# Kernel tuning notes

Measured on AMD Instinct MI355X. Metric: run time of the kernel, lower is better.

## Reference

```python
import jax, jax.numpy as jnp
import numpy as np

LORA_SCALE = 0.5
LAYER_IDX = 0
NUM_ADAPTERS = 8

def setup_inputs() -> dict:
    key = jax.random.key(0)
    ks = jax.random.split(key, 11)
    T, H, I, A, L, R = 2048, 4096, 11008, NUM_ADAPTERS, 1, 16
    s_base = 1.0 / np.sqrt(H)
    s_down = 1.0 / np.sqrt(I)
    return {
        "x": jax.random.normal(ks[0], (T, H), jnp.float32),
        "gate_w": jax.random.normal(ks[1], (I, H), jnp.float32) * s_base,
        "up_w": jax.random.normal(ks[2], (I, H), jnp.float32) * s_base,
        "down_w": jax.random.normal(ks[3], (H, I), jnp.float32) * s_down,
        "gate_wa": jax.random.normal(ks[4], (A, L, R, H), jnp.float32) * s_base,
        "gate_wb": jax.random.normal(ks[5], (A, L, I, R), jnp.float32) * 0.01,
        "up_wa": jax.random.normal(ks[6], (A, L, R, H), jnp.float32) * s_base,
        "up_wb": jax.random.normal(ks[7], (A, L, I, R), jnp.float32) * 0.01,
        "down_wa": jax.random.normal(ks[8], (A, L, R, I), jnp.float32) * s_down,
        "down_wb": jax.random.normal(ks[9], (A, L, H, R), jnp.float32) * 0.01,
        "indices": jax.random.randint(ks[10], (T,), 0, A, jnp.int64),
    }

def _add_lora(y, x_in, wa, wb, idx, scale):
    # wa: [A, L, r, in], wb: [A, L, out, r]; per-token adapter gather (BGMV)
    wa_t = wa[idx, LAYER_IDX]          # [T, r, in]
    wb_t = wb[idx, LAYER_IDX]          # [T, out, r]
    v = jnp.einsum('ti,tri->tr', x_in, wa_t)     # [T, r]
    return y + scale * jnp.einsum('tr,tor->to', v, wb_t)

def reference(x, gate_w, up_w, down_w, gate_wa, gate_wb, up_wa, up_wb, down_wa, down_wb, indices):
    gate = x @ gate_w.T                                   # [T, I]
    gate = _add_lora(gate, x, gate_wa, gate_wb, indices, LORA_SCALE)
    gate = jax.nn.silu(gate)
    up = x @ up_w.T                                       # [T, I]
    up = _add_lora(up, x, up_wa, up_wb, indices, LORA_SCALE)
    t = gate * up                                         # [T, I]
    down = t @ down_w.T                                   # [T, H]
    down = _add_lora(down, t, down_wa, down_wb, indices, LORA_SCALE)
    return down
```

## Files before the change

### kernel.cpp

```cpp
#include <hip/hip_runtime.h>
#include <hip/hip_bf16.h>
#include <cstdint>


#define T_TOK 2048
#define H_DIM 4096
#define I_DIM 11008
#define R_LORA 16
#define KA1 4352
#define KA2 11136
#define N_STK 22016

typedef __bf16 bf16x8 __attribute__((ext_vector_type(8)));
typedef float f32x4 __attribute__((ext_vector_type(4)));

__device__ __forceinline__ float bf2f(unsigned short u) {
    union { unsigned int i; float f; } v;
    v.i = ((unsigned int)u) << 16;
    return v.f;
}
__device__ __forceinline__ unsigned short f2bf(float f) {
    __bf16 b = (__bf16)f;
    unsigned short u;
    __builtin_memcpy(&u, &b, 2);
    return u;
}
__device__ __forceinline__ void cvt8(const float* s, unsigned short* d) {
    float4 a = reinterpret_cast<const float4*>(s)[0];
    float4 b = reinterpret_cast<const float4*>(s)[1];
    uint4 o;
    o.x = (unsigned)f2bf(a.x) | ((unsigned)f2bf(a.y) << 16);
    o.y = (unsigned)f2bf(a.z) | ((unsigned)f2bf(a.w) << 16);
    o.z = (unsigned)f2bf(b.x) | ((unsigned)f2bf(b.y) << 16);
    o.w = (unsigned)f2bf(b.z) | ((unsigned)f2bf(b.w) << 16);
    *reinterpret_cast<uint4*>(d) = o;
}
__device__ __forceinline__ void gload_lds16(const void* g, void* l) {
    __builtin_amdgcn_global_load_lds(
        (const __attribute__((address_space(1))) void*)g,
        (__attribute__((address_space(3))) void*)l,
        16, 0, 0);
}

__global__ __launch_bounds__(256) void cvt_rows(
    const float* __restrict__ src, unsigned short* __restrict__ dst, int K)
{
    const int row = blockIdx.x;
    const int tid = threadIdx.x;
    const float* s = src + (size_t)row * K;
    unsigned short* d = dst + (size_t)row * K;
    for (int k = tid * 8; k < K; k += 256 * 8) cvt8(s + k, d + k);
}

__global__ __launch_bounds__(256) void build_xa_x(
    const float* __restrict__ x, unsigned short* __restrict__ xa)
{
    const int t = blockIdx.x;
    const int tid = threadIdx.x;
    const float* s = x + (size_t)t * H_DIM;
    unsigned short* d = xa + (size_t)t * KA1;
    for (int k = tid * 8; k < H_DIM; k += 2048) cvt8(s + k, d + k);
}

__global__ __launch_bounds__(256) void fill_xa_aug(
    const float* __restrict__ P, const int* __restrict__ idx,
    unsigned short* __restrict__ xa)
{
    const int t = blockIdx.x;
    const int tid = threadIdx.x;
    const int a = (tid & 127) >> 4;
    float v = 0.f;
    if (a == idx[t]) {
        #pragma unroll
        for (int s = 0; s < 4; ++s)
            v += P[((size_t)s * T_TOK + t) * 256 + tid];
        v *= 0.5f;
    }
    xa[(size_t)t * KA1 + H_DIM + tid] = f2bf(v);
}

__global__ __launch_bounds__(128) void fill_ta(
    const float* __restrict__ P, const int* __restrict__ idx,
    unsigned short* __restrict__ t_aug)
{
    const int t = blockIdx.x;
    const int tid = threadIdx.x;
    const int a = tid >> 4;
    float v = 0.f;
    if (a == idx[t]) {
        #pragma unroll
        for (int s = 0; s < 4; ++s)
            v += P[((size_t)s * T_TOK + t) * 128 + tid];
        v *= 0.5f;
    }
    t_aug[(size_t)t * KA2 + I_DIM + tid] = f2bf(v);
}

__global__ __launch_bounds__(256) void build_w_aug(
    const float* __restrict__ w, const float* __restrict__ wb,
    unsigned short* __restrict__ dst,
    int Nrows, int Ksrc, int Kdst, int self_off, int zero_off)
{
    const int c = blockIdx.x;
    const int tid = threadIdx.x;
    const float* src = w + (size_t)c * Ksrc;
    unsigned short* d = dst + (size_t)c * Kdst;
    for (int k = tid * 8; k < Ksrc; k += 256 * 8) cvt8(src + k, d + k);
    if (tid < 128) {
        const int a = tid >> 4, r = tid & 15;
        const float v = wb[(((size_t)a * Nrows) + c) * R_LORA + r];
        d[self_off + tid] = f2bf(v);
        if (zero_off >= 0) d[zero_off + tid] = 0;
    }
}

__global__ __launch_bounds__(256) void silu_mul(
    const unsigned short* __restrict__ C, unsigned short* __restrict__ T)
{
    const long long nv = (long long)T_TOK * (I_DIM / 8);
    long long i = (long long)blockIdx.x * 256 + threadIdx.x;
    const long long stride = (long long)gridDim.x * 256;
    for (; i < nv; i += stride) {
        const int t = (int)(i / (I_DIM / 8));
        const int c8 = (int)(i % (I_DIM / 8)) * 8;
        const unsigned short* g = C + (size_t)t * N_STK + c8;
        uint4 gv = *reinterpret_cast<const uint4*>(g);
        uint4 uv = *reinterpret_cast<const uint4*>(g + I_DIM);
        const unsigned short* gp = reinterpret_cast<const unsigned short*>(&gv);
        const unsigned short* up = reinterpret_cast<const unsigned short*>(&uv);
        unsigned short og[8];
        #pragma unroll
        for (int e = 0; e < 8; ++e) {
            const float gf = bf2f(gp[e]);
            const float uf = bf2f(up[e]);
            og[e] = f2bf(uf * gf / (1.f + __expf(-gf)));
        }
        *reinterpret_cast<uint4*>(T + (size_t)t * KA2 + c8) =
            *reinterpret_cast<const uint4*>(og);
    }
}

__global__ __launch_bounds__(256) void add_inplace(
    float* __restrict__ out, const float* __restrict__ p)
{
    const long long n4 = (long long)T_TOK * H_DIM / 4;
    long long i = (long long)blockIdx.x * 256 + threadIdx.x;
    const long long stride = (long long)gridDim.x * 256;
    for (; i < n4; i += stride) {
        float4 a = reinterpret_cast<float4*>(out)[i];
        float4 b = reinterpret_cast<const float4*>(p)[i];
        a.x += b.x; a.y += b.y; a.z += b.z; a.w += b.w;
        reinterpret_cast<float4*>(out)[i] = a;
    }
}

__global__ __launch_bounds__(512) void gemm_thin_sk(
    const unsigned short* __restrict__ A, int lda,
    const unsigned short* __restrict__ B, int ldb,
    float* __restrict__ P, int N, int K)
{
    __shared__ __align__(16) unsigned short As[128][64];
    __shared__ __align__(16) unsigned short Bs[128][64];

    const int tid = threadIdx.x;
    const int lane = tid & 63;
    const int wid = tid >> 6;
    const int wr = wid >> 2;
    const int wc = wid & 3;
    const int fr = lane & 15;
    const int hi = lane >> 4;
    const int fsw = fr & 7;

    const int bm0 = blockIdx.y * 128;
    const int bn0 = blockIdx.x * 128;
    const int ks = K / 4;
    const int k0 = blockIdx.z * ks;
    float* out = P + (size_t)blockIdx.z * T_TOK * N;

    const int srow = tid >> 3;
    const int sslot = tid & 7;
    const int gcol = (sslot ^ (srow & 7)) * 8;
    const unsigned short* Ag = A + (size_t)(bm0 + srow) * lda + gcol;
    const unsigned short* Bg = B + (size_t)(bn0 + srow) * ldb + gcol;
    const size_t halfA = (size_t)64 * lda;
    const size_t halfB = (size_t)64 * ldb;

    f32x4 acc[4][2] = {};

    for (int kt = k0; kt < k0 + ks; kt += 64) {
        gload_lds16(Ag + kt,         &As[srow][sslot * 8]);
        gload_lds16(Ag + halfA + kt, &As[64 + srow][sslot * 8]);
        gload_lds16(Bg + kt,         &Bs[srow][sslot * 8]);
        gload_lds16(Bg + halfB + kt, &Bs[64 + srow][sslot * 8]);
        __syncthreads();
        #pragma unroll
        for (int kk = 0; kk < 2; ++kk) {
            bf16x8 a_[4], b_[2];
            #pragma unroll
            for (int m = 0; m < 4; ++m)
                a_[m] = *reinterpret_cast<const bf16x8*>(
                    &As[wr * 64 + m * 16 + fr][((kk * 4 + hi) ^ fsw) * 8]);
            #pragma unroll
            for (int n = 0; n < 2; ++n)
                b_[n] = *reinterpret_cast<const bf16x8*>(
                    &Bs[wc * 32 + n * 16 + fr][((kk * 4 + hi) ^ fsw) * 8]);
            #pragma unroll
            for (int m = 0; m < 4; ++m)
                #pragma unroll
                for (int n = 0; n < 2; ++n)
                    acc[m][n] = __builtin_amdgcn_mfma_f32_16x16x32_bf16(
                        a_[m], b_[n], acc[m][n], 0, 0, 0);
        }
        __syncthreads();
    }

    const int orow0 = bm0 + wr * 64 + hi * 4;
    const int ocol0 = bn0 + wc * 32 + fr;
    #pragma unroll
    for (int m = 0; m < 4; ++m)
        #pragma unroll
        for (int j = 0; j < 4; ++j) {
            const int row = orow0 + m * 16 + j;
            #pragma unroll
            for (int n = 0; n < 2; ++n)
                out[(size_t)row * N + ocol0 + n * 16] = acc[m][n][j];
        }
}

#define RD_A(BUF, MH)                                                         \
    do {                                                                      \
        _Pragma("unroll")                                                     \
        for (int mq = 0; mq < 4; ++mq) {                                      \
            _Pragma("unroll")                                                 \
            for (int k = 0; k < 2; ++k)                                       \
                a_[mq][k] = *reinterpret_cast<const bf16x8*>(                 \
                    &lds[BUF][wr * 128 + (MH) * 64 + mq * 16 + fr]            \
                        [((k * 4 + hi) ^ fsw) * 8]);                          \
        }                                                                     \
    } while (0)

#define RD_B(BUF, NH, DST)                                                    \
    do {                                                                      \
        _Pragma("unroll")                                                     \
        for (int nq = 0; nq < 2; ++nq) {                                      \
            _Pragma("unroll")                                                 \
            for (int k = 0; k < 2; ++k)                                       \
                DST[nq][k] = *reinterpret_cast<const bf16x8*>(                \
                    &lds[BUF][256 + wc * 64 + (NH) * 32 + nq * 16 + fr]       \
                        [((k * 4 + hi) ^ fsw) * 8]);                          \
        }                                                                     \
    } while (0)

#define MM(MH, NH, BSRC)                                                      \
    do {                                                                      \
        _Pragma("unroll")                                                     \
        for (int mq = 0; mq < 4; ++mq) {                                      \
            _Pragma("unroll")                                                 \
            for (int nq = 0; nq < 2; ++nq) {                                  \
                _Pragma("unroll")                                             \
                for (int k = 0; k < 2; ++k)                                   \
                    acc[(MH) * 4 + mq][(NH) * 2 + nq] =                       \
                        __builtin_amdgcn_mfma_f32_16x16x32_bf16(              \
                            a_[mq][k], BSRC[nq][k],                           \
                            acc[(MH) * 4 + mq][(NH) * 2 + nq], 0, 0, 0);      \
            }                                                                 \
        }                                                                     \
    } while (0)

template <int MODE>
__global__ __launch_bounds__(512, 2) void gemmk(
    const unsigned short* __restrict__ A, int lda,
    const unsigned short* __restrict__ B, int ldb,
    int nks_in,
    unsigned short* __restrict__ outb, int ldob,
    float* __restrict__ outf0, float* __restrict__ outf1)
{
    __shared__ __align__(16) unsigned short lds[2][512][64];

    const int tid = threadIdx.x;
    const int lane = tid & 63;
    const int wid = tid >> 6;
    const int wr = wid >> 2;
    const int wc = wid & 3;
    const int fr = lane & 15;
    const int hi = lane >> 4;
    const int fsw = fr & 7;

    int bm, bn, koff = 0, nks = nks_in;
    float* outf = outf0;
    if constexpr (MODE == 2) {
        bm = blockIdx.x & 7;
        bn = (blockIdx.x >> 3) & 15;
        nks = 87;
        if (blockIdx.x >> 7) { koff = 87 * 64; outf = outf1; }
    } else {
        bm = blockIdx.x & 7;
        bn = blockIdx.x >> 3;
    }
    const int bm0 = bm * 256;
    const int bn0 = bn * 256;

    const int srow = tid >> 3;
    const int sslot = tid & 7;
    const int gcol = (sslot ^ (srow & 7)) * 8;
    const unsigned short* Ap = A + (size_t)(bm0 + srow) * lda + gcol + koff;
    const unsigned short* Bp = B + (size_t)(bn0 + srow) * ldb + gcol + koff;

    f32x4 acc[8][4] = {};
    bf16x8 a_[4][2], b0_[2][2], b1_[2][2];

    auto stage = [&](int buf, int kt) {
        #pragma unroll
        for (int q = 0; q < 4; ++q)
            gload_lds16(Ap + (size_t)(q * 64) * lda + kt,
                        &lds[buf][q * 64 + srow][sslot * 8]);
        #pragma unroll
        for (int q = 0; q < 4; ++q)
            gload_lds16(Bp + (size_t)(q * 64) * ldb + kt,
                        &lds[buf][256 + q * 64 + srow][sslot * 8]);
    };

    stage(0, 0);
    __syncthreads();

    for (int t = 0; t < nks; ++t) {
        const int cur = t & 1;
        if (t + 1 < nks) stage(cur ^ 1, (t + 1) * 64);

        RD_A(cur, 0);
        RD_B(cur, 0, b0_);
        MM(0, 0, b0_);
        RD_B(cur, 1, b1_);
        MM(0, 1, b1_);
        RD_A(cur, 1);
        MM(1, 0, b0_);
        MM(1, 1, b1_);

        __syncthreads();
    }

    const int orow0 = bm0 + wr * 128 + hi * 4;
    const int ocol0 = bn0 + wc * 64 + fr;
    #pragma unroll
    for (int m = 0; m < 8; ++m) {
        #pragma unroll
        for (int jj = 0; jj < 4; ++jj) {
            const int row = orow0 + m * 16 + jj;
            #pragma unroll
            for (int n = 0; n < 4; ++n) {
                const int col = ocol0 + n * 16;
                if constexpr (MODE == 0) {
                    outb[(size_t)row * ldob + col] = f2bf(acc[m][n][jj]);
                } else if constexpr (MODE == 1) {
                    const float g = bf2f(outb[(size_t)row * ldob + col]);
                    const float u = acc[m][n][jj];
                    outb[(size_t)row * ldob + col] =
                        f2bf(u * g / (1.f + __expf(-g)));
                } else {
                    outf[(size_t)row * H_DIM + col] = acc[m][n][jj];
                }
            }
        }
    }
}

extern "C" void kernel_launch(void* const* d_in, const int* in_sizes, int n_in,
                              void* d_out, int out_size, void* d_ws, size_t ws_size,
                              hipStream_t stream)
{
    const float* x       = (const float*)d_in[0];
    const float* gate_w  = (const float*)d_in[1];
    const float* up_w    = (const float*)d_in[2];
    const float* down_w  = (const float*)d_in[3];
    const float* gate_wa = (const float*)d_in[4];
    const float* gate_wb = (const float*)d_in[5];
    const float* up_wa   = (const float*)d_in[6];
    const float* up_wb   = (const float*)d_in[7];
    const float* down_wa = (const float*)d_in[8];
    const float* down_wb = (const float*)d_in[9];
    const int*   indices = (const int*)d_in[10];
    float* out = (float*)d_out;

    char* ws = (char*)d_ws;
    size_t off = 0;
    auto alloc = [&](size_t bytes) {
        char* p = ws + off;
        off += (bytes + 255) & ~(size_t)255;
        return p;
    };
    unsigned short* xa     = (unsigned short*)alloc((size_t)T_TOK * KA1 * 2);
    unsigned short* wg_aug = (unsigned short*)alloc((size_t)I_DIM * KA1 * 2);
    unsigned short* wu_aug = (unsigned short*)alloc((size_t)I_DIM * KA1 * 2);
    unsigned short* t_aug  = (unsigned short*)alloc((size_t)T_TOK * KA2 * 2);
    unsigned short* wab_gu = (unsigned short*)alloc((size_t)256 * H_DIM * 2);
    const size_t base_need = off;
    const size_t c_need = ((size_t)T_TOK * N_STK * 2 + 255) & ~(size_t)255;
    const bool stacked = (ws_size >= base_need + c_need);
    unsigned short* Cbuf = stacked ? (unsigned short*)alloc(c_need) : nullptr;

    float* Pgu = (float*)(t_aug);
    float* Pd  = stacked ? (float*)Cbuf
                         : (float*)(t_aug + (size_t)T_TOK * KA2) - (size_t)T_TOK * 128 * 4;
    unsigned short* wd_aug = wu_aug;
    unsigned short* wab_d  = wu_aug + (size_t)H_DIM * KA2;
    float* partial1 = (float*)wg_aug;

    cvt_rows<<<128, 256, 0, stream>>>(gate_wa, wab_gu, H_DIM);
    cvt_rows<<<128, 256, 0, stream>>>(up_wa, wab_gu + (size_t)128 * H_DIM, H_DIM);
    build_xa_x<<<T_TOK, 256, 0, stream>>>(x, xa);
    gemm_thin_sk<<<dim3(2, 16, 4), 512, 0, stream>>>(xa, KA1, wab_gu, H_DIM, Pgu, 256, H_DIM);
    fill_xa_aug<<<T_TOK, 256, 0, stream>>>(Pgu, indices, xa);

    build_w_aug<<<I_DIM, 256, 0, stream>>>(gate_w, gate_wb, wg_aug,
                                           I_DIM, H_DIM, KA1, H_DIM, H_DIM + 128);
    build_w_aug<<<I_DIM, 256, 0, stream>>>(up_w, up_wb, wu_aug,
                                           I_DIM, H_DIM, KA1, H_DIM + 128, H_DIM);

    if (stacked) {
        gemmk<0><<<8 * (N_STK / 256), 512, 0, stream>>>(
            xa, KA1, wg_aug, KA1, KA1 / 64, Cbuf, N_STK, nullptr, nullptr);
        silu_mul<<<2048, 256, 0, stream>>>(Cbuf, t_aug);
    } else {
        gemmk<0><<<8 * (I_DIM / 256), 512, 0, stream>>>(
            xa, KA1, wg_aug, KA1, KA1 / 64, t_aug, KA2, nullptr, nullptr);
        gemmk<1><<<8 * (I_DIM / 256), 512, 0, stream>>>(
            xa, KA1, wu_aug, KA1, KA1 / 64, t_aug, KA2, nullptr, nullptr);
    }

    cvt_rows<<<128, 256, 0, stream>>>(down_wa, wab_d, I_DIM);
    gemm_thin_sk<<<dim3(1, 16, 4), 512, 0, stream>>>(t_aug, KA2, wab_d, I_DIM, Pd, 128, I_DIM);
    fill_ta<<<T_TOK, 128, 0, stream>>>(Pd, indices, t_aug);
    build_w_aug<<<H_DIM, 256, 0, stream>>>(down_w, down_wb, wd_aug,
                                           H_DIM, I_DIM, KA2, I_DIM, -1);

    gemmk<2><<<256, 512, 0, stream>>>(
        t_aug, KA2, wd_aug, KA2, 0, nullptr, 0, out, partial1);
    add_inplace<<<2048, 256, 0, stream>>>(out, partial1);

    (void)in_sizes; (void)n_in; (void)out_size; (void)ws_size;
}
```

Measured before the change: 837.4 us.

## Interleave gate/up weight rows and fuse SiLU-multiply into GEMM epilogue

Gate and up weight rows are interleaved into one stacked B matrix so each output column pair (gate, up) lands in adjacent lanes. The GEMM epilogue exchanges the pair with a lane shuffle and writes silu(gate)*up directly into t_aug. This removes the stacked bf16 intermediate buffer, the separate silu_mul pass and one of the two weight-build launches. The down-projection split-K block mapping is also remapped per XCD, and the workspace layout is reworked. Half the lanes sit idle during the epilogue store, and the stores are strided.

After: 816.2 us. -2.5%, faster.

```diff
diff --git a/kernel.cpp b/kernel.cpp
--- a/kernel.cpp
+++ b/kernel.cpp
@@ -96,10 +96,31 @@
     t_aug[(size_t)t * KA2 + I_DIM + tid] = f2bf(v);
 }
 
+__global__ __launch_bounds__(256) void build_w_int(
+    const float* __restrict__ gw, const float* __restrict__ uw,
+    const float* __restrict__ gwb, const float* __restrict__ uwb,
+    unsigned short* __restrict__ dst)
+{
+    const int c = blockIdx.x;
+    const int i = c >> 1;
+    const int par = c & 1;
+    const int tid = threadIdx.x;
+    const float* src = (par ? uw : gw) + (size_t)i * H_DIM;
+    const float* wb  = (par ? uwb : gwb);
+    unsigned short* d = dst + (size_t)c * KA1;
+    for (int k = tid * 8; k < H_DIM; k += 256 * 8) cvt8(src + k, d + k);
+    if (tid < 128) {
+        const int a = tid >> 4, r = tid & 15;
+        const float v = wb[(((size_t)a * I_DIM) + i) * R_LORA + r];
+        d[H_DIM + par * 128 + tid] = f2bf(v);
+        d[H_DIM + (1 - par) * 128 + tid] = 0;
+    }
+}
+
 __global__ __launch_bounds__(256) void build_w_aug(
     const float* __restrict__ w, const float* __restrict__ wb,
     unsigned short* __restrict__ dst,
-    int Nrows, int Ksrc, int Kdst, int self_off, int zero_off)
+    int Nrows, int Ksrc, int Kdst, int self_off)
 {
     const int c = blockIdx.x;
     const int tid = threadIdx.x;
@@ -110,33 +131,6 @@
         const int a = tid >> 4, r = tid & 15;
         const float v = wb[(((size_t)a * Nrows) + c) * R_LORA + r];
         d[self_off + tid] = f2bf(v);
-        if (zero_off >= 0) d[zero_off + tid] = 0;
-    }
-}
-
-__global__ __launch_bounds__(256) void silu_mul(
-    const unsigned short* __restrict__ C, unsigned short* __restrict__ T)
-{
-    const long long nv = (long long)T_TOK * (I_DIM / 8);
-    long long i = (long long)blockIdx.x * 256 + threadIdx.x;
-    const long long stride = (long long)gridDim.x * 256;
-    for (; i < nv; i += stride) {
-        const int t = (int)(i / (I_DIM / 8));
-        const int c8 = (int)(i % (I_DIM / 8)) * 8;
-        const unsigned short* g = C + (size_t)t * N_STK + c8;
-        uint4 gv = *reinterpret_cast<const uint4*>(g);
-        uint4 uv = *reinterpret_cast<const uint4*>(g + I_DIM);
-        const unsigned short* gp = reinterpret_cast<const unsigned short*>(&gv);
-        const unsigned short* up = reinterpret_cast<const unsigned short*>(&uv);
-        unsigned short og[8];
-        #pragma unroll
-        for (int e = 0; e < 8; ++e) {
-            const float gf = bf2f(gp[e]);
-            const float uf = bf2f(up[e]);
-            og[e] = f2bf(uf * gf / (1.f + __expf(-gf)));
-        }
-        *reinterpret_cast<uint4*>(T + (size_t)t * KA2 + c8) =
-            *reinterpret_cast<const uint4*>(og);
     }
 }
 
@@ -272,7 +266,7 @@
     const unsigned short* __restrict__ A, int lda,
     const unsigned short* __restrict__ B, int ldb,
     int nks_in,
-    unsigned short* __restrict__ outb, int ldob,
+    unsigned short* __restrict__ outb,
     float* __restrict__ outf0, float* __restrict__ outf1)
 {
     __shared__ __align__(16) unsigned short lds[2][512][64];
@@ -289,10 +283,12 @@
     int bm, bn, koff = 0, nks = nks_in;
     float* outf = outf0;
     if constexpr (MODE == 2) {
-        bm = blockIdx.x & 7;
-        bn = (blockIdx.x >> 3) & 15;
+        const int xcd = blockIdx.x & 7;
+        const int c = blockIdx.x >> 3;
+        bm = (xcd >> 1) * 2 + (c & 1);
+        bn = (xcd & 1) * 8 + ((c >> 1) & 7);
         nks = 87;
-        if (blockIdx.x >> 7) { koff = 87 * 64; outf = outf1; }
+        if (c >> 4) { koff = 87 * 64; outf = outf1; }
     } else {
         bm = blockIdx.x & 7;
         bn = blockIdx.x >> 3;
@@ -348,16 +344,16 @@
             const int row = orow0 + m * 16 + jj;
             #pragma unroll
             for (int n = 0; n < 4; ++n) {
-                const int col = ocol0 + n * 16;
-                if constexpr (MODE == 0) {
-                    outb[(size_t)row * ldob + col] = f2bf(acc[m][n][jj]);
-                } else if constexpr (MODE == 1) {
-                    const float g = bf2f(outb[(size_t)row * ldob + col]);
-                    const float u = acc[m][n][jj];
-                    outb[(size_t)row * ldob + col] =
-                        f2bf(u * g / (1.f + __expf(-g)));
+                if constexpr (MODE == 3) {
+                    const float v = acc[m][n][jj];
+                    const float w = __shfl_xor(v, 1);
+                    if ((fr & 1) == 0) {
+                        const float sg = v / (1.f + __expf(-v));
+                        const int s = ocol0 + n * 16;
+                        outb[(size_t)row * KA2 + (s >> 1)] = f2bf(sg * w);
+                    }
                 } else {
-                    outf[(size_t)row * H_DIM + col] = acc[m][n][jj];
+                    outf[(size_t)row * H_DIM + ocol0 + n * 16] = acc[m][n][jj];
                 }
             }
         }
@@ -388,22 +384,16 @@
         off += (bytes + 255) & ~(size_t)255;
         return p;
     };
-    unsigned short* xa     = (unsigned short*)alloc((size_t)T_TOK * KA1 * 2);
-    unsigned short* wg_aug = (unsigned short*)alloc((size_t)I_DIM * KA1 * 2);
-    unsigned short* wu_aug = (unsigned short*)alloc((size_t)I_DIM * KA1 * 2);
-    unsigned short* t_aug  = (unsigned short*)alloc((size_t)T_TOK * KA2 * 2);
+    unsigned short* xa    = (unsigned short*)alloc((size_t)T_TOK * KA1 * 2);
+    unsigned short* wB    = (unsigned short*)alloc((size_t)N_STK * KA1 * 2);
+    unsigned short* t_aug = (unsigned short*)alloc((size_t)T_TOK * KA2 * 2);
     unsigned short* wab_gu = (unsigned short*)alloc((size_t)256 * H_DIM * 2);
-    const size_t base_need = off;
-    const size_t c_need = ((size_t)T_TOK * N_STK * 2 + 255) & ~(size_t)255;
-    const bool stacked = (ws_size >= base_need + c_need);
-    unsigned short* Cbuf = stacked ? (unsigned short*)alloc(c_need) : nullptr;
-
-    float* Pgu = (float*)(t_aug);
-    float* Pd  = stacked ? (float*)Cbuf
-                         : (float*)(t_aug + (size_t)T_TOK * KA2) - (size_t)T_TOK * 128 * 4;
-    unsigned short* wd_aug = wu_aug;
-    unsigned short* wab_d  = wu_aug + (size_t)H_DIM * KA2;
-    float* partial1 = (float*)wg_aug;
+
+    float* Pgu = (float*)t_aug;
+    float* Pd  = (float*)xa;
+    unsigned short* wd_aug = wB;
+    unsigned short* wab_d  = wB + (size_t)H_DIM * KA2;
+    float* partial1 = (float*)(wab_d + (size_t)128 * I_DIM + 64);
 
     cvt_rows<<<128, 256, 0, stream>>>(gate_wa, wab_gu, H_DIM);
     cvt_rows<<<128, 256, 0, stream>>>(up_wa, wab_gu + (size_t)128 * H_DIM, H_DIM);
@@ -411,30 +401,19 @@
     gemm_thin_sk<<<dim3(2, 16, 4), 512, 0, stream>>>(xa, KA1, wab_gu, H_DIM, Pgu, 256, H_DIM);
     fill_xa_aug<<<T_TOK, 256, 0, stream>>>(Pgu, indices, xa);
 
-    build_w_aug<<<I_DIM, 256, 0, stream>>>(gate_w, gate_wb, wg_aug,
-                                           I_DIM, H_DIM, KA1, H_DIM, H_DIM + 128);
-    build_w_aug<<<I_DIM, 256, 0, stream>>>(up_w, up_wb, wu_aug,
-                                           I_DIM, H_DIM, KA1, H_DIM + 128, H_DIM);
-
-    if (stacked) {
-        gemmk<0><<<8 * (N_STK / 256), 512, 0, stream>>>(
-            xa, KA1, wg_aug, KA1, KA1 / 64, Cbuf, N_STK, nullptr, nullptr);
-        silu_mul<<<2048, 256, 0, stream>>>(Cbuf, t_aug);
-    } else {
-        gemmk<0><<<8 * (I_DIM / 256), 512, 0, stream>>>(
-            xa, KA1, wg_aug, KA1, KA1 / 64, t_aug, KA2, nullptr, nullptr);
-        gemmk<1><<<8 * (I_DIM / 256), 512, 0, stream>>>(
-            xa, KA1, wu_aug, KA1, KA1 / 64, t_aug, KA2, nullptr, nullptr);
-    }
+    build_w_int<<<N_STK, 256, 0, stream>>>(gate_w, up_w, gate_wb, up_wb, wB);
+
+    gemmk<3><<<8 * (N_STK / 256), 512, 0, stream>>>(
+        xa, KA1, wB, KA1, KA1 / 64, t_aug, nullptr, nullptr);
 
     cvt_rows<<<128, 256, 0, stream>>>(down_wa, wab_d, I_DIM);
     gemm_thin_sk<<<dim3(1, 16, 4), 512, 0, stream>>>(t_aug, KA2, wab_d, I_DIM, Pd, 128, I_DIM);
     fill_ta<<<T_TOK, 128, 0, stream>>>(Pd, indices, t_aug);
     build_w_aug<<<H_DIM, 256, 0, stream>>>(down_w, down_wb, wd_aug,
-                                           H_DIM, I_DIM, KA2, I_DIM, -1);
+                                           H_DIM, I_DIM, KA2, I_DIM);
 
     gemmk<2><<<256, 512, 0, stream>>>(
-        t_aug, KA2, wd_aug, KA2, 0, nullptr, 0, out, partial1);
+        t_aug, KA2, wd_aug, KA2, 0, nullptr, out, partial1);
     add_inplace<<<2048, 256, 0, stream>>>(out, partial1);
 
     (void)in_sizes; (void)n_in; (void)out_size; (void)ws_size;
```
